# Optimization experiments

Hardware: AMD Instinct MI355X
Metric: run time of the kernel (lower is better)

The kernel has to match this reference:

```python
import jax, jax.numpy as jnp
import numpy as np

BN, S, D = 200, 128, 1024          # B*N entity rows, scenes, d_model
D_INNER, D_STATE, D_CONV = 2048, 32, 4


def setup_inputs() -> dict:
    key = jax.random.key(0)
    ks = jax.random.split(key, 8)
    s = 0.02
    return {
        "x": jax.random.normal(ks[0], (BN, S, D), jnp.float32),
        "emotion_bias": jax.random.uniform(ks[1], (BN, S, 1), jnp.float32),
        "norm_w": jnp.ones((D,), jnp.float32),
        "norm_b": jnp.zeros((D,), jnp.float32),
        "in_proj_W": jax.random.normal(ks[2], (2 * D_INNER, D), jnp.float32) * s,
        "conv_w": jax.random.normal(ks[3], (D_INNER, 1, D_CONV), jnp.float32) * 0.1,
        "conv_b": jnp.zeros((D_INNER,), jnp.float32),
        "x_proj_W": jax.random.normal(ks[4], (2 * D_STATE + 1, D_INNER), jnp.float32) * s,
        "dt_W": jax.random.normal(ks[5], (D_INNER, 1), jnp.float32),
        "dt_b": jnp.zeros((D_INNER,), jnp.float32),
        "out_W": jax.random.normal(ks[6], (D, D_INNER), jnp.float32) * s,
        "emotion_scale": jnp.array(0.1, jnp.float32),
    }


def reference(x, emotion_bias, norm_w, norm_b, in_proj_W, conv_w, conv_b,
              x_proj_W, dt_W, dt_b, out_W, emotion_scale):
    residual = x
    # LayerNorm (eps=1e-5, biased variance as in torch)
    mu = x.mean(-1, keepdims=True)
    var = ((x - mu) ** 2).mean(-1, keepdims=True)
    xn = (x - mu) * jax.lax.rsqrt(var + 1e-5) * norm_w + norm_b

    xz = xn @ in_proj_W.T                      # [BN, S, 2*d_inner]
    x_in, z = jnp.split(xz, 2, axis=-1)

    # causal depthwise conv1d (torch pads d_conv-1 both sides, truncates to S == left-pad only)
    xc = jax.lax.conv_general_dilated(
        x_in.transpose(0, 2, 1), conv_w,
        window_strides=(1,), padding=[(D_CONV - 1, 0)],
        feature_group_count=D_INNER,
        dimension_numbers=("NCH", "OIH", "NCH"))
    xc = (xc + conv_b[None, :, None]).transpose(0, 2, 1)   # [BN, S, d_inner]
    x_act = jax.nn.silu(xc)

    x_ssm = x_act @ x_proj_W.T                 # [BN, S, 2*d_state+1]
    delta_raw, B_mat, C = jnp.split(x_ssm, [1, 1 + D_STATE], axis=-1)
    delta = jax.nn.softplus(delta_raw @ dt_W.T + dt_b)     # [BN, S, d_inner]
    delta = jnp.maximum(delta + emotion_scale * emotion_bias, 1e-4)

    def step(h, inp):
        d_t, B_t, C_t, xa_t = inp              # [BN,d_inner],[BN,n],[BN,n],[BN,d_inner]
        h = h * jnp.exp(-d_t)[..., None] + B_t[:, None, :] * xa_t[..., None]
        h = jnp.clip(h, -100.0, 100.0)
        y_t = jnp.einsum("bdn,bn->bd", h, C_t)
        return h, y_t

    h0 = jnp.zeros((BN, D_INNER, D_STATE), jnp.float32)
    xs = (delta.transpose(1, 0, 2), B_mat.transpose(1, 0, 2),
          C.transpose(1, 0, 2), x_act.transpose(1, 0, 2))
    _, y = jax.lax.scan(step, h0, xs)          # y: [S, BN, d_inner]
    y = y.transpose(1, 0, 2)

    return (y * jax.nn.silu(z)) @ out_W.T + residual
```

## Files before the change

kernel.cpp:

```cpp
#include <hip/hip_runtime.h>
#include <cstdint>
#include <cstddef>

#define NBN   200
#define NS    128
#define ND    1024
#define NDI   2048
#define NST   32
#define NROWS (NBN * NS)

typedef __attribute__((ext_vector_type(8))) short bf16x8;
typedef __attribute__((ext_vector_type(4))) float f32x4;

__device__ __forceinline__ unsigned short f2bf(float f) {
    unsigned int u = __float_as_uint(f);
    u += 0x7fffu + ((u >> 16) & 1u);
    return (unsigned short)(u >> 16);
}
__device__ __forceinline__ float bf2f(unsigned short h) {
    return __uint_as_float(((unsigned int)h) << 16);
}

__device__ __forceinline__ void gl_lds16(const void* g, void* l) {
    typedef __attribute__((address_space(1))) const unsigned int* gp_t;
    typedef __attribute__((address_space(3))) unsigned int* lp_t;
    __builtin_amdgcn_global_load_lds((gp_t)(uintptr_t)g,
                                     (lp_t)(unsigned int)(uintptr_t)l, 16, 0, 0);
}

__global__ __launch_bounds__(256) void cvt_kernel(const float* __restrict__ src,
                                                  unsigned short* __restrict__ dst, int n) {
    int i = blockIdx.x * 256 + threadIdx.x;
    if (i < n) dst[i] = f2bf(src[i]);
}

__global__ __launch_bounds__(256) void padwx_kernel(const float* __restrict__ src,
                                                    unsigned short* __restrict__ dst) {
    int i = blockIdx.x * 256 + threadIdx.x;
    int r = i >> 11;
    dst[i] = (r < 65) ? f2bf(src[i]) : (unsigned short)0;
}

__global__ __launch_bounds__(256) void ln_kernel(const float* __restrict__ x,
                                                 const float* __restrict__ gw,
                                                 const float* __restrict__ gb,
                                                 unsigned short* __restrict__ xn) {
    __shared__ float ss[4], ss2[4];
    size_t row = blockIdx.x;
    int tid = threadIdx.x;
    const float4* px = (const float4*)(x + row * ND);
    float4 v = px[tid];
    float s  = v.x + v.y + v.z + v.w;
    float s2 = fmaf(v.x, v.x, fmaf(v.y, v.y, fmaf(v.z, v.z, v.w * v.w)));
    #pragma unroll
    for (int off = 32; off > 0; off >>= 1) {
        s  += __shfl_down(s,  off, 64);
        s2 += __shfl_down(s2, off, 64);
    }
    if ((tid & 63) == 0) { ss[tid >> 6] = s; ss2[tid >> 6] = s2; }
    __syncthreads();
    float tot  = ss[0] + ss[1] + ss[2] + ss[3];
    float tot2 = ss2[0] + ss2[1] + ss2[2] + ss2[3];
    float mu   = tot * (1.f / ND);
    float var  = fmaf(tot2, 1.f / ND, -mu * mu);
    float rstd = rsqrtf(var + 1e-5f);
    float4 wv = ((const float4*)gw)[tid];
    float4 bv = ((const float4*)gb)[tid];
    ushort4 o;
    o.x = f2bf(fmaf((v.x - mu) * rstd, wv.x, bv.x));
    o.y = f2bf(fmaf((v.y - mu) * rstd, wv.y, bv.y));
    o.z = f2bf(fmaf((v.z - mu) * rstd, wv.z, bv.z));
    o.w = f2bf(fmaf((v.w - mu) * rstd, wv.w, bv.w));
    ((ushort4*)(xn + row * ND))[tid] = o;
}


#define BARRIER __builtin_amdgcn_s_barrier()
#define LGKM0  asm volatile("s_waitcnt lgkmcnt(0)" ::: "memory")
#define VMCNT6 asm volatile("s_waitcnt vmcnt(6)" ::: "memory")
#define VMCNT0 asm volatile("s_waitcnt vmcnt(0)" ::: "memory")
#define NOWAIT ((void)0)
#define PRIO1  __builtin_amdgcn_s_setprio(1)
#define PRIO0  __builtin_amdgcn_s_setprio(0)

#define STG_A(t, kp) {                                                        \
    gl_lds16(gA0 + (size_t)(t) * 64 + (kp) * 32,                              \
             lA + (((t) & 1) << 15) + ((kp) << 14));                          \
    gl_lds16(gA1 + (size_t)(t) * 64 + (kp) * 32,                              \
             lA + (((t) & 1) << 15) + ((kp) << 14) + 8192); }
#define STG_B(t, kp) {                                                        \
    gl_lds16(gB0 + (size_t)(t) * 64 + (kp) * 32,                              \
             lB + (((t) & 1) << 15) + ((kp) << 14));                          \
    gl_lds16(gB1 + (size_t)(t) * 64 + (kp) * 32,                              \
             lB + (((t) & 1) << 15) + ((kp) << 14) + 8192); }

#define RD_A(dst, mh, kp) { _Pragma("unroll")                                 \
    for (int mi = 0; mi < 4; ++mi)                                            \
        dst[mi] = *(const bf16x8*)(aRd + bo + (kp) * 16384 + (mh) * 4096 + mi * 1024); }
#define RD_B(dst, kp) { _Pragma("unroll")                                     \
    for (int ni = 0; ni < 4; ++ni)                                            \
        dst[ni] = *(const bf16x8*)(bRd + bo + (kp) * 16384 + ni * 1024); }

#define MM(mh, AV, BV) { _Pragma("unroll")                                    \
    for (int mi = 0; mi < 4; ++mi) { _Pragma("unroll")                        \
        for (int ni = 0; ni < 4; ++ni)                                        \
            acc[(mh) * 4 + mi][ni] = __builtin_amdgcn_mfma_f32_16x16x32_bf16( \
                AV[mi], BV[ni], acc[(mh) * 4 + mi][ni], 0, 0, 0); } }

#define TILE(t, DO_AP1, DO_T2, W) {                                           \
    const int bo = ((t) & 1) << 15;                                           \
    RD_A(aK0, 0, 0); RD_B(bK0, 0);                                            \
    if (DO_AP1) STG_A((t) + 1, 1);                                            \
    BARRIER; LGKM0; PRIO1; MM(0, aK0, bK0); PRIO0; BARRIER;                   \
    RD_A(aK1, 0, 1); RD_B(bK1, 1);                                            \
    if (DO_T2) STG_B((t) + 2, 0);                                             \
    BARRIER; LGKM0; PRIO1; MM(0, aK1, bK1); PRIO0; BARRIER;                   \
    RD_A(aK0, 1, 0);                                                          \
    if (DO_T2) STG_B((t) + 2, 1);                                             \
    BARRIER; LGKM0; PRIO1; MM(1, aK0, bK0); PRIO0; BARRIER;                   \
    RD_A(aK1, 1, 1);                                                          \
    if (DO_T2) STG_A((t) + 2, 0);                                             \
    BARRIER; LGKM0; PRIO1; MM(1, aK1, bK1); PRIO0;                            \
    W;                                                                        \
    BARRIER; }

template <int K, int EPI>
__global__ __launch_bounds__(512, 2)
void gemm256(const unsigned short* __restrict__ A,
             const unsigned short* __restrict__ B,
             int N, void* __restrict__ outp, const float* __restrict__ resid) {
    constexpr int NT = K / 64;
    static_assert(NT >= 3, "need >=3 K-tiles");
    __shared__ __align__(16) char smem[131072];

    const int tid  = threadIdx.x;
    const int lane = tid & 63;
    const int wid  = tid >> 6;
    const int lrow = lane & 15;
    const int kq   = lane >> 4;
    const int wmi  = wid >> 2;
    const int wni  = wid & 3;

    const int gx  = gridDim.x;
    const int nwg = gx * gridDim.y;
    const int lin = blockIdx.y * gx + blockIdx.x;
    const int id2 = (lin & 7) * (nwg >> 3) + (lin >> 3);
    const int bm  = id2 % gx;
    const int bn  = id2 / gx;

    const size_t m0 = (size_t)bm * 256;
    const size_t n0 = (size_t)bn * 256;

    const int fr = (lrow >> 1) & 3;
    const char* aRd = smem +          (wmi * 128 + lrow) * 64 + ((kq ^ fr) << 4);
    const char* bRd = smem + 65536 + (wni * 64  + lrow) * 64 + ((kq ^ fr) << 4);

    const int srow = wid * 16 + (lane >> 2);
    const int scol = (((lane & 3) ^ ((lane >> 3) & 3)) << 3);
    const unsigned short* gA0 = A + (m0 + srow) * K + scol;
    const unsigned short* gA1 = A + (m0 + 128 + srow) * K + scol;
    const unsigned short* gB0 = B + (n0 + srow) * K + scol;
    const unsigned short* gB1 = B + (n0 + 128 + srow) * K + scol;
    char* lA = smem + wid * 1024;
    char* lB = smem + 65536 + wid * 1024;

    f32x4 acc[8][4];
    #pragma unroll
    for (int i = 0; i < 8; ++i)
        #pragma unroll
        for (int j = 0; j < 4; ++j) acc[i][j] = (f32x4){0.f, 0.f, 0.f, 0.f};

    bf16x8 aK0[4], aK1[4], bK0[4], bK1[4];

    STG_B(0, 0); STG_B(0, 1); STG_A(0, 0); STG_A(0, 1);
    STG_B(1, 0); STG_B(1, 1); STG_A(1, 0);
    VMCNT6;
    BARRIER;

    int t = 0;
    #pragma unroll 2
    for (; t < NT - 2; ++t) { TILE(t, 1, 1, VMCNT6); }
    TILE((NT - 2), 1, 0, VMCNT0);
    TILE((NT - 1), 0, 0, NOWAIT);

    #pragma unroll
    for (int mi = 0; mi < 8; ++mi)
        #pragma unroll
        for (int ni = 0; ni < 4; ++ni)
            #pragma unroll
            for (int r = 0; r < 4; ++r) {
                size_t row = m0 + wmi * 128 + mi * 16 + kq * 4 + r;
                size_t col = n0 + wni * 64 + ni * 16 + lrow;
                size_t idx = row * (size_t)N + col;
                float v = acc[mi][ni][r];
                if (EPI == 0) ((unsigned short*)outp)[idx] = f2bf(v);
                else          ((float*)outp)[idx] = v + resid[idx];
            }
}

__global__ __launch_bounds__(256) void conv_silu_kernel(const unsigned short* __restrict__ xz,
                                                        const float* __restrict__ cw,
                                                        const float* __restrict__ cb,
                                                        unsigned short* __restrict__ xact) {
    int tid = blockIdx.x * 256 + threadIdx.x;
    int c = tid & (NDI - 1);
    int b = tid >> 11;
    float4 wv = ((const float4*)cw)[c];
    float w0 = wv.x, w1 = wv.y, w2 = wv.z, w3 = wv.w;
    float bias = cb[c];
    const unsigned short* px = xz + (size_t)b * NS * (2 * NDI) + c;
    unsigned short* po = xact + (size_t)b * NS * NDI + c;
    float x0 = 0.f, x1 = 0.f, x2 = 0.f;
    for (int t = 0; t < NS; t++) {
        float x3 = bf2f(px[(size_t)t * (2 * NDI)]);
        float v  = fmaf(x3, w3, fmaf(x2, w2, fmaf(x1, w1, fmaf(x0, w0, bias))));
        float s  = v * __builtin_amdgcn_rcpf(1.f + __expf(-v));
        po[(size_t)t * NDI] = f2bf(s);
        x0 = x1; x1 = x2; x2 = x3;
    }
}

__global__ __launch_bounds__(256, 2)
void gemm2_kernel(const unsigned short* __restrict__ A,
                  const unsigned short* __restrict__ B,
                  float* __restrict__ out) {
    __shared__ __align__(16) unsigned short As[64 * 32];
    __shared__ __align__(16) unsigned short Bs[80 * 32];
    const int tid  = threadIdx.x;
    const int bm   = blockIdx.x;
    const int wid  = tid >> 6;
    const int lane = tid & 63;
    const int lrow = lane & 15;
    const int kq   = lane >> 4;

    f32x4 acc[5];
    #pragma unroll
    for (int i = 0; i < 5; i++) acc[i] = (f32x4){0.f, 0.f, 0.f, 0.f};

    const int r1 = tid >> 2;
    const int c8 = (tid & 3) << 3;
    const unsigned short* gA1 = A + ((size_t)bm * 64 + r1) * NDI + c8;
    const unsigned short* gB1 = B + (size_t)r1 * NDI + c8;
    const unsigned short* gB2 = B + (size_t)(64 + r1) * NDI + c8;
    char* lA1 = (char*)As + wid * 1024;
    char* lB1 = (char*)Bs + wid * 1024;
    char* lB2 = (char*)Bs + 4096;

    for (int kt = 0; kt < NDI; kt += 32) {
        __syncthreads();
        gl_lds16(gA1, lA1);
        gl_lds16(gB1, lB1);
        if (tid < 64) gl_lds16(gB2, lB2);
        gA1 += 32; gB1 += 32; gB2 += 32;
        __syncthreads();
        bf16x8 af = *(const bf16x8*)&As[(wid * 16 + lrow) * 32 + kq * 8];
        #pragma unroll
        for (int ni = 0; ni < 5; ni++) {
            bf16x8 bfr = *(const bf16x8*)&Bs[(ni * 16 + lrow) * 32 + kq * 8];
            acc[ni] = __builtin_amdgcn_mfma_f32_16x16x32_bf16(af, bfr, acc[ni], 0, 0, 0);
        }
    }
    #pragma unroll
    for (int ni = 0; ni < 5; ni++)
        #pragma unroll
        for (int r = 0; r < 4; r++) {
            size_t row = (size_t)bm * 64 + wid * 16 + kq * 4 + r;
            int col = ni * 16 + lrow;
            out[row * 80 + col] = acc[ni][r];
        }
}

__global__ __launch_bounds__(256, 2)
void ssd_kernel(const float* __restrict__ xssm,
                unsigned short* xact_g,
                const unsigned short* __restrict__ xz,
                const float* __restrict__ dtW,
                const float* __restrict__ dtb,
                const float* __restrict__ eb,
                const float* __restrict__ es_p) {
    __shared__ float sDR[32], sDE[32];
    __shared__ __align__(16) unsigned short sC[32][32];
    __shared__ __align__(16) unsigned short sB[32][32];
    __shared__ __align__(16) unsigned short sBt[32][32];
    __shared__ __align__(16) unsigned short sG[32][32];
    __shared__ __align__(16) unsigned short sP[256][32];
    __shared__ __align__(16) float          sE[256][32];
    __shared__ __align__(16) unsigned short sH[256][32];

    const int tid  = threadIdx.x;
    const int b    = blockIdx.y;
    const int d0   = blockIdx.x * 256;
    const int lane = tid & 63;
    const int wid  = tid >> 6;
    const int lrow = lane & 15;
    const int kq   = lane >> 4;
    const int wd0  = wid * 64;

    const float w  = dtW[d0 + tid];
    const float bb = dtb[d0 + tid];
    const float es = es_p[0];

    for (int i = tid; i < 256 * 32; i += 256) ((unsigned short*)sH)[i] = 0;

    #pragma unroll 1
    for (int c = 0; c < 4; ++c) {
        __syncthreads();
        {
            const float* src = xssm + ((size_t)b * 128 + c * 32) * 80;
            for (int i = tid; i < 2560; i += 256) {
                int t = i / 80, col = i - t * 80;
                float v = src[i];
                if (col == 0) sDR[t] = v;
                else if (col < 33) {
                    unsigned short bv = f2bf(v);
                    sB[t][col - 1] = bv;
                    sBt[col - 1][t] = bv;
                } else if (col < 65) sC[t][col - 33] = f2bf(v);
            }
            if (tid < 32) sDE[tid] = es * eb[b * 128 + c * 32 + tid];
        }
        __syncthreads();

        {
            int mi = wid >> 1, ni = wid & 1;
            bf16x8 af = *(const bf16x8*)&sC[mi * 16 + lrow][kq * 8];
            bf16x8 bf = *(const bf16x8*)&sB[ni * 16 + lrow][kq * 8];
            f32x4 z4 = (f32x4){0.f, 0.f, 0.f, 0.f};
            f32x4 g = __builtin_amdgcn_mfma_f32_16x16x32_bf16(af, bf, z4, 0, 0, 0);
            #pragma unroll
            for (int r = 0; r < 4; ++r) {
                int t = mi * 16 + kq * 4 + r, s = ni * 16 + lrow;
                float val = (s <= t) ? g[r] : 0.f;
                *(unsigned short*)((char*)sG + t * 64 +
                    ((((s >> 3) ^ (t & 3)) << 4) | ((s & 7) << 1))) = f2bf(val);
            }
        }

        {
            const unsigned short* pxa =
                xact_g + ((size_t)b * 128 + c * 32) * 2048 + d0 + tid;
            float L = 0.f;
            for (int t8 = 0; t8 < 4; ++t8) {
                bf16x8 pv;
                #pragma unroll
                for (int j = 0; j < 8; ++j) {
                    int t = t8 * 8 + j;
                    float raw = fmaf(sDR[t], w, bb);
                    float sp  = (raw > 20.f) ? raw : __logf(1.f + __expf(raw));
                    float delta = fmaxf(sp + sDE[t], 1e-4f);
                    L += delta;
                    float xa = bf2f(pxa[(size_t)t * 2048]);
                    pv[j] = (short)f2bf(xa * __expf(L));
                    *(float*)((char*)sE + tid * 128 +
                        ((((t >> 2) ^ (tid & 7)) << 4) | ((t & 3) << 2))) = __expf(-L);
                }
                *(bf16x8*)((char*)sP + tid * 64 + (((t8 ^ (tid & 3)) << 4))) = pv;
            }
        }
        __syncthreads();

        f32x4 acc[2][4], racc[2][4];
        bf16x8 cfrag[2], gfrag[2], btfrag[2], hfrag[4], pfrag[4];
        #pragma unroll
        for (int mi = 0; mi < 2; ++mi) {
            int tr = mi * 16 + lrow;
            cfrag[mi]  = *(const bf16x8*)&sC[tr][kq * 8];
            gfrag[mi]  = *(const bf16x8*)((const char*)sG + tr * 64 +
                                          (((kq ^ (tr & 3)) << 4)));
            btfrag[mi] = *(const bf16x8*)&sBt[tr][kq * 8];
        }
        #pragma unroll
        for (int ni = 0; ni < 4; ++ni) {
            int dc = wd0 + ni * 16 + lrow;
            hfrag[ni] = *(const bf16x8*)&sH[dc][kq * 8];
            pfrag[ni] = *(const bf16x8*)((const char*)sP + dc * 64 +
                                         (((kq ^ (dc & 3)) << 4)));
        }
        #pragma unroll
        for (int mi = 0; mi < 2; ++mi)
            #pragma unroll
            for (int ni = 0; ni < 4; ++ni) {
                f32x4 z4 = (f32x4){0.f, 0.f, 0.f, 0.f};
                acc[mi][ni] = __builtin_amdgcn_mfma_f32_16x16x32_bf16(
                    cfrag[mi], hfrag[ni], z4, 0, 0, 0);
                acc[mi][ni] = __builtin_amdgcn_mfma_f32_16x16x32_bf16(
                    gfrag[mi], pfrag[ni], acc[mi][ni], 0, 0, 0);
                racc[mi][ni] = __builtin_amdgcn_mfma_f32_16x16x32_bf16(
                    btfrag[mi], pfrag[ni], z4, 0, 0, 0);
            }

        #pragma unroll
        for (int mi = 0; mi < 2; ++mi)
            #pragma unroll
            for (int ni = 0; ni < 4; ++ni) {
                int dc = wd0 + ni * 16 + lrow;
                f32x4 ev = *(const f32x4*)((const char*)sE + dc * 128 +
                                           ((((mi * 4 + kq) ^ (dc & 7)) << 4)));
                size_t rowg = (size_t)b * 128 + c * 32 + mi * 16 + kq * 4;
                #pragma unroll
                for (int r = 0; r < 4; ++r) {
                    float y  = acc[mi][ni][r] * ev[r];
                    float zz = bf2f(xz[(rowg + r) * 4096 + 2048 + d0 + dc]);
                    float sig = __builtin_amdgcn_rcpf(1.f + __expf(-zz));
                    xact_g[(rowg + r) * 2048 + d0 + dc] = f2bf(y * zz * sig);
                }
            }

        #pragma unroll
        for (int ni = 0; ni < 4; ++ni) {
            int dc = wd0 + ni * 16 + lrow;
            float e31 = *(const float*)((const char*)sE + dc * 128 +
                                        (((7 ^ (dc & 7)) << 4) | 12));
            #pragma unroll
            for (int mi = 0; mi < 2; ++mi)
                #pragma unroll
                for (int r = 0; r < 4; ++r) {
                    int n = mi * 16 + kq * 4 + r;
                    float h = bf2f(sH[dc][n]) + racc[mi][ni][r];
                    sH[dc][n] = f2bf(e31 * h);
                }
        }
    }
}

extern "C" void kernel_launch(void* const* d_in, const int* in_sizes, int n_in,
                              void* d_out, int out_size, void* d_ws, size_t ws_size,
                              hipStream_t stream) {
    const float* x   = (const float*)d_in[0];
    const float* eb  = (const float*)d_in[1];
    const float* nw  = (const float*)d_in[2];
    const float* nb  = (const float*)d_in[3];
    const float* Wi  = (const float*)d_in[4];
    const float* cw  = (const float*)d_in[5];
    const float* cb  = (const float*)d_in[6];
    const float* Wx  = (const float*)d_in[7];
    const float* dtW = (const float*)d_in[8];
    const float* dtb = (const float*)d_in[9];
    const float* Wo  = (const float*)d_in[10];
    const float* es  = (const float*)d_in[11];
    float* out = (float*)d_out;

    char* ws = (char*)d_ws;
    unsigned short* wi_b   = (unsigned short*)(ws + 0);
    unsigned short* wo_b   = (unsigned short*)(ws + 8388608);
    unsigned short* wx_b   = (unsigned short*)(ws + 12582912);
    unsigned short* xz_b   = (unsigned short*)(ws + 12910592);
    unsigned short* xact_b = (unsigned short*)(ws + 222625792);
    float*          xssm   = (float*)(ws + 327483392);
    if (ws_size < (size_t)335675392) return;

    cvt_kernel<<<(2 * NDI * ND + 255) / 256, 256, 0, stream>>>(Wi, wi_b, 2 * NDI * ND);
    cvt_kernel<<<(ND * NDI + 255) / 256, 256, 0, stream>>>(Wo, wo_b, ND * NDI);
    padwx_kernel<<<(80 * NDI) / 256, 256, 0, stream>>>(Wx, wx_b);

    unsigned short* xn_b = xact_b;
    ln_kernel<<<NROWS, 256, 0, stream>>>(x, nw, nb, xn_b);

    gemm256<ND, 0><<<dim3(NROWS / 256, (2 * NDI) / 256), 512, 0, stream>>>(
        xn_b, wi_b, 2 * NDI, xz_b, nullptr);

    conv_silu_kernel<<<(NBN * NDI) / 256, 256, 0, stream>>>(xz_b, cw, cb, xact_b);

    gemm2_kernel<<<NROWS / 64, 256, 0, stream>>>(xact_b, wx_b, xssm);

    ssd_kernel<<<dim3(NDI / 256, NBN), 256, 0, stream>>>(xssm, xact_b, xz_b, dtW, dtb, eb, es);

    gemm256<NDI, 1><<<dim3(NROWS / 256, ND / 256), 512, 0, stream>>>(
        xact_b, wo_b, ND, out, x);
}
```

Baseline: 882.4 us.

## Fuse causal conv+SiLU and z-gate SiLU into in_proj GEMM epilogue

The in_proj GEMM epilogue now stages each wave's bf16 tile in LDS transposed by channel and applies the causal depthwise conv and SiLU along the 128-step sequence. Each 256-row block corresponds to exactly two entities, so the conv window never crosses a tile boundary. The z half gets SiLU applied in the epilogue and is stored compactly, so the SSD kernel reads a pre-activated 2048-wide z instead of recomputing the sigmoid. This removes the separate conv kernel and the full xz round-trip through memory. The cost is a longer, serial per-lane epilogue with strided stores, and the output GEMM now uses nontemporal loads and stores.

```diff
diff --git a/kernel.cpp b/kernel.cpp
--- a/kernel.cpp
+++ b/kernel.cpp
@@ -128,7 +128,9 @@
 __global__ __launch_bounds__(512, 2)
 void gemm256(const unsigned short* __restrict__ A,
              const unsigned short* __restrict__ B,
-             int N, void* __restrict__ outp, const float* __restrict__ resid) {
+             int N, void* __restrict__ outp, const float* __restrict__ resid,
+             const float* __restrict__ cw, const float* __restrict__ cb,
+             unsigned short* __restrict__ out2) {
     constexpr int NT = K / 64;
     static_assert(NT >= 3, "need >=3 K-tiles");
     __shared__ __align__(16) char smem[131072];
@@ -183,40 +185,70 @@
     TILE((NT - 2), 1, 0, VMCNT0);
     TILE((NT - 1), 0, 0, NOWAIT);
 
-    #pragma unroll
-    for (int mi = 0; mi < 8; ++mi)
-        #pragma unroll
-        for (int ni = 0; ni < 4; ++ni)
-            #pragma unroll
-            for (int r = 0; r < 4; ++r) {
-                size_t row = m0 + wmi * 128 + mi * 16 + kq * 4 + r;
-                size_t col = n0 + wni * 64 + ni * 16 + lrow;
-                size_t idx = row * (size_t)N + col;
-                float v = acc[mi][ni][r];
-                if (EPI == 0) ((unsigned short*)outp)[idx] = f2bf(v);
-                else          ((float*)outp)[idx] = v + resid[idx];
-            }
-}
-
-__global__ __launch_bounds__(256) void conv_silu_kernel(const unsigned short* __restrict__ xz,
-                                                        const float* __restrict__ cw,
-                                                        const float* __restrict__ cb,
-                                                        unsigned short* __restrict__ xact) {
-    int tid = blockIdx.x * 256 + threadIdx.x;
-    int c = tid & (NDI - 1);
-    int b = tid >> 11;
-    float4 wv = ((const float4*)cw)[c];
-    float w0 = wv.x, w1 = wv.y, w2 = wv.z, w3 = wv.w;
-    float bias = cb[c];
-    const unsigned short* px = xz + (size_t)b * NS * (2 * NDI) + c;
-    unsigned short* po = xact + (size_t)b * NS * NDI + c;
-    float x0 = 0.f, x1 = 0.f, x2 = 0.f;
-    for (int t = 0; t < NS; t++) {
-        float x3 = bf2f(px[(size_t)t * (2 * NDI)]);
-        float v  = fmaf(x3, w3, fmaf(x2, w2, fmaf(x1, w1, fmaf(x0, w0, bias))));
-        float s  = v * __builtin_amdgcn_rcpf(1.f + __expf(-v));
-        po[(size_t)t * NDI] = f2bf(s);
-        x0 = x1; x1 = x2; x2 = x3;
+    if (EPI == 1) {
+        #pragma unroll
+        for (int mi = 0; mi < 8; ++mi)
+            #pragma unroll
+            for (int ni = 0; ni < 4; ++ni)
+                #pragma unroll
+                for (int r = 0; r < 4; ++r) {
+                    size_t row = m0 + wmi * 128 + mi * 16 + kq * 4 + r;
+                    size_t col = n0 + wni * 64 + ni * 16 + lrow;
+                    size_t idx = row * (size_t)N + col;
+                    float v = acc[mi][ni][r] + __builtin_nontemporal_load(&resid[idx]);
+                    __builtin_nontemporal_store(v, &((float*)outp)[idx]);
+                }
+    } else {
+        BARRIER;
+        if (n0 < 2048) {
+            char* wb = smem + wid * 16384;
+            #pragma unroll
+            for (int mi = 0; mi < 8; ++mi)
+                #pragma unroll
+                for (int ni = 0; ni < 4; ++ni) {
+                    int cl = ni * 16 + lrow;
+                    int slot = mi * 2 + (kq >> 1);
+                    ushort4 pk;
+                    pk.x = f2bf(acc[mi][ni][0]); pk.y = f2bf(acc[mi][ni][1]);
+                    pk.z = f2bf(acc[mi][ni][2]); pk.w = f2bf(acc[mi][ni][3]);
+                    *(ushort4*)(wb + cl * 256 +
+                                (((slot ^ lrow) << 4) | ((kq & 1) << 3))) = pk;
+                }
+            LGKM0;
+            __builtin_amdgcn_sched_barrier(0);
+            const int ch = (int)n0 + wni * 64 + lane;
+            float4 wv = ((const float4*)cw)[ch];
+            float bias = cb[ch];
+            float x0 = 0.f, x1 = 0.f, x2 = 0.f;
+            unsigned short* po = (unsigned short*)outp + (m0 + wmi * 128) * NDI + ch;
+            const char* rb = wb + lane * 256;
+            const int cx = lane & 15;
+            for (int s = 0; s < 16; ++s) {
+                bf16x8 v = *(const bf16x8*)(rb + ((s ^ cx) << 4));
+                #pragma unroll
+                for (int j = 0; j < 8; ++j) {
+                    float x3 = bf2f((unsigned short)v[j]);
+                    float vv = fmaf(x3, wv.w, fmaf(x2, wv.z,
+                               fmaf(x1, wv.y, fmaf(x0, wv.x, bias))));
+                    float sg = vv * __builtin_amdgcn_rcpf(1.f + __expf(-vv));
+                    po[(size_t)(s * 8 + j) * NDI] = f2bf(sg);
+                    x0 = x1; x1 = x2; x2 = x3;
+                }
+            }
+        } else {
+            #pragma unroll
+            for (int mi = 0; mi < 8; ++mi)
+                #pragma unroll
+                for (int ni = 0; ni < 4; ++ni)
+                    #pragma unroll
+                    for (int r = 0; r < 4; ++r) {
+                        size_t row = m0 + wmi * 128 + mi * 16 + kq * 4 + r;
+                        size_t col = (n0 - 2048) + wni * 64 + ni * 16 + lrow;
+                        float v = acc[mi][ni][r];
+                        float sg = v * __builtin_amdgcn_rcpf(1.f + __expf(-v));
+                        __builtin_nontemporal_store(f2bf(sg), &out2[row * 2048 + col]);
+                    }
+        }
     }
 }
 
@@ -273,7 +305,7 @@
 __global__ __launch_bounds__(256, 2)
 void ssd_kernel(const float* __restrict__ xssm,
                 unsigned short* xact_g,
-                const unsigned short* __restrict__ xz,
+                const unsigned short* __restrict__ zs,
                 const float* __restrict__ dtW,
                 const float* __restrict__ dtb,
                 const float* __restrict__ eb,
@@ -399,10 +431,9 @@
                 size_t rowg = (size_t)b * 128 + c * 32 + mi * 16 + kq * 4;
                 #pragma unroll
                 for (int r = 0; r < 4; ++r) {
+                    size_t gi = (rowg + r) * 2048 + d0 + dc;
                     float y  = acc[mi][ni][r] * ev[r];
-                    float zz = bf2f(xz[(rowg + r) * 4096 + 2048 + d0 + dc]);
-                    float sig = __builtin_amdgcn_rcpf(1.f + __expf(-zz));
-                    xact_g[(rowg + r) * 2048 + d0 + dc] = f2bf(y * zz * sig);
+                    xact_g[gi] = f2bf(y * bf2f(zs[gi]));
                 }
             }
 
@@ -444,27 +475,25 @@
     unsigned short* wi_b   = (unsigned short*)(ws + 0);
     unsigned short* wo_b   = (unsigned short*)(ws + 8388608);
     unsigned short* wx_b   = (unsigned short*)(ws + 12582912);
-    unsigned short* xz_b   = (unsigned short*)(ws + 12910592);
-    unsigned short* xact_b = (unsigned short*)(ws + 222625792);
-    float*          xssm   = (float*)(ws + 327483392);
-    if (ws_size < (size_t)335675392) return;
+    unsigned short* zs_b   = (unsigned short*)(ws + 12910592);
+    unsigned short* xn_b   = (unsigned short*)(ws + 117768192);
+    unsigned short* xact_b = (unsigned short*)(ws + 170196992);
+    float*          xssm   = (float*)(ws + 275054592);
+    if (ws_size < (size_t)283246592) return;
 
     cvt_kernel<<<(2 * NDI * ND + 255) / 256, 256, 0, stream>>>(Wi, wi_b, 2 * NDI * ND);
     cvt_kernel<<<(ND * NDI + 255) / 256, 256, 0, stream>>>(Wo, wo_b, ND * NDI);
     padwx_kernel<<<(80 * NDI) / 256, 256, 0, stream>>>(Wx, wx_b);
 
-    unsigned short* xn_b = xact_b;
     ln_kernel<<<NROWS, 256, 0, stream>>>(x, nw, nb, xn_b);
 
-    gemm256<ND, 0><<<dim3(NROWS / 256, (2 * NDI) / 256), 512, 0, stream>>>(
-        xn_b, wi_b, 2 * NDI, xz_b, nullptr);
-
-    conv_silu_kernel<<<(NBN * NDI) / 256, 256, 0, stream>>>(xz_b, cw, cb, xact_b);
+    gemm256<ND, 2><<<dim3(NROWS / 256, (2 * NDI) / 256), 512, 0, stream>>>(
+        xn_b, wi_b, 2 * NDI, xact_b, nullptr, cw, cb, zs_b);
 
     gemm2_kernel<<<NROWS / 64, 256, 0, stream>>>(xact_b, wx_b, xssm);
 
-    ssd_kernel<<<dim3(NDI / 256, NBN), 256, 0, stream>>>(xssm, xact_b, xz_b, dtW, dtb, eb, es);
+    ssd_kernel<<<dim3(NDI / 256, NBN), 256, 0, stream>>>(xssm, xact_b, zs_b, dtW, dtb, eb, es);
 
     gemm256<NDI, 1><<<dim3(NROWS / 256, ND / 256), 512, 0, stream>>>(
-        xact_b, wo_b, ND, out, x);
-}
+        xact_b, wo_b, ND, out, x, nullptr, nullptr, nullptr);
+}
```

After: 866.9 us. No clear change (-1.8%).
